# Kernel optimization log

Measured on AMD Instinct MI355X. Metric: run time of the kernel, lower is better.

The kernel has to match this reference:

```python
import jax, jax.numpy as jnp
import numpy as np

B, H = 2048, 1024
P_DROP = 0.6


def setup_inputs() -> dict:
    key = jax.random.key(0)
    ks = jax.random.split(key, 17)
    stdv = 1.0 / np.sqrt(H)
    u = lambda k, shape: jax.random.uniform(k, shape, jnp.float32, -stdv, stdv)
    inp = {
        'input': jax.random.normal(ks[0], (B, H), jnp.float32),
        'hidden': jax.random.normal(ks[1], (B, H), jnp.float32),
        'pre_cell': jax.random.normal(ks[2], (B, H), jnp.float32),
        # weights are (hidden_size, input_size) and used as input @ W (requires H == input_size)
        'w_i': u(ks[3], (H, H)), 'w_f': u(ks[4], (H, H)),
        'w_o': u(ks[5], (H, H)), 'w_c': u(ks[6], (H, H)),
        'u_i': u(ks[7], (H, H)), 'u_f': u(ks[8], (H, H)),
        'u_o': u(ks[9], (H, H)), 'u_c': u(ks[10], (H, H)),
        'bias1': u(ks[11], (H,)), 'bias2': u(ks[12], (H,)),
        'bias3': u(ks[13], (H,)), 'bias4': u(ks[14], (H,)),
    }
    # F.dropout(training=True) mask, pre-scaled by 1/(1-p); shape matches h_t [B,1,H]
    keep = jax.random.bernoulli(ks[15], 1.0 - P_DROP, (B, 1, H))
    inp['drop_mask'] = keep.astype(jnp.float32) / (1.0 - P_DROP)
    return inp


def reference(input, hidden, pre_cell, w_i, w_f, w_o, w_c, u_i, u_f, u_o, u_c,
              bias1, bias2, bias3, bias4, drop_mask):
    # Fuse the 8 small GEMMs into 2 big ones: gate order (f, i, o, c)
    Wx = jnp.concatenate([w_f, w_i, w_o, w_c], axis=1)   # [H, 4H]
    Wh = jnp.concatenate([u_f, u_i, u_o, u_c], axis=1)   # [H, 4H]
    b = jnp.concatenate([bias1, bias2, bias3, bias4])    # [4H]
    gates = input @ Wx + hidden @ Wh + b                 # [B, 4H]
    f_t, i_t, o_t, g_t = jnp.split(gates, 4, axis=1)
    f_t = jax.nn.sigmoid(f_t)
    i_t = jax.nn.sigmoid(i_t)
    o_t = jax.nn.sigmoid(o_t)
    g_t = jnp.tanh(g_t)
    c_t = pre_cell * f_t + i_t * g_t                     # [B, H]
    h_t = o_t * jnp.tanh(c_t)                            # [B, H]
    h_t = h_t[:, None, :] * drop_mask                    # dropout (training=True)
    c_t = c_t[:, None, :]
    return h_t, c_t
```

## Files before the change

### kernel.cpp

```cpp
#include <hip/hip_runtime.h>
#include <hip/hip_bf16.h>
#include <cstdint>

#define B_DIM 2048
#define H_DIM 1024
#define K_DIM 2048
#define N_DIM 4096

typedef unsigned short u16;
typedef __attribute__((ext_vector_type(8))) short bf16x8;
typedef __attribute__((ext_vector_type(8))) unsigned short u16x8;
typedef __attribute__((ext_vector_type(4))) float f32x4;

__device__ __forceinline__ u16 f2bf(float f) {
    unsigned int u = __float_as_uint(f);
    u += 0x7FFFu + ((u >> 16) & 1u);
    return (u16)(u >> 16);
}

__device__ __forceinline__ float sigmoid_f(float x) {
    return 1.0f / (1.0f + __expf(-x));
}

__device__ __forceinline__ float tanh_f(float x) {
    float e = __expf(2.0f * x);
    return 1.0f - 2.0f / (e + 1.0f);
}

__device__ __forceinline__ void async16(const u16* g, u16* l) {
    __builtin_amdgcn_global_load_lds(
        (const __attribute__((address_space(1))) unsigned int*)g,
        (__attribute__((address_space(3))) unsigned int*)l,
        16, 0, 0);
}

__global__ __launch_bounds__(256) void pack_all(
    const float* __restrict__ input, const float* __restrict__ hidden,
    const float* __restrict__ w_f, const float* __restrict__ w_i,
    const float* __restrict__ w_o, const float* __restrict__ w_c,
    const float* __restrict__ u_f, const float* __restrict__ u_i,
    const float* __restrict__ u_o, const float* __restrict__ u_c,
    const float* __restrict__ b1, const float* __restrict__ b2,
    const float* __restrict__ b3, const float* __restrict__ b4,
    u16* __restrict__ A, u16* __restrict__ Bt, float* __restrict__ bias_il) {
    __shared__ float tile[32][65];
    const int blk = blockIdx.x;
    const int t = threadIdx.x;

    if (blk < 4096) {
        int idx = (blk * 256 + t) * 4;
        int m = idx >> 11;
        int k = idx & (K_DIM - 1);
        const float* src = (k < H_DIM) ? (input + (size_t)m * H_DIM + k)
                                       : (hidden + (size_t)m * H_DIM + (k - H_DIM));
        float4 v = *(const float4*)src;
        ushort4 o;
        o.x = f2bf(v.x); o.y = f2bf(v.y); o.z = f2bf(v.z); o.w = f2bf(v.w);
        *(ushort4*)(A + idx) = o;
    } else if (blk < 8192) {
        int b2i = blk - 4096;
        int z = b2i >> 9;
        int rem = b2i & 511;
        int hx = rem & 31;
        int ky = rem >> 5;
        const float* M;
        switch (z) {
            case 0: M = w_f; break;
            case 1: M = w_i; break;
            case 2: M = w_o; break;
            case 3: M = w_c; break;
            case 4: M = u_f; break;
            case 5: M = u_i; break;
            case 6: M = u_o; break;
            default: M = u_c; break;
        }
        const int g = z & 3;
        const int half = z >> 2;
        const int h0 = hx * 32;
        const int k0 = ky * 64;
#pragma unroll
        for (int it = 0; it < 2; it++) {
            int kl = (t >> 3) + it * 32;
            int hl = (t & 7) * 4;
            float4 v = *(const float4*)(M + (size_t)(k0 + kl) * H_DIM + h0 + hl);
            tile[hl + 0][kl] = v.x;
            tile[hl + 1][kl] = v.y;
            tile[hl + 2][kl] = v.z;
            tile[hl + 3][kl] = v.w;
        }
        __syncthreads();
        int hl = t >> 3;
        int ko = (t & 7) * 8;
        u16x8 o;
#pragma unroll
        for (int q = 0; q < 8; q++) o[q] = f2bf(tile[hl][ko + q]);
        size_t n = 4 * (size_t)(h0 + hl) + g;
        *(u16x8*)(Bt + n * K_DIM + half * H_DIM + k0 + ko) = o;
    } else {
        int idx = (blk - 8192) * 256 + t;
        int h = idx >> 2, g = idx & 3;
        const float* b = (g == 0) ? b1 : (g == 1) ? b2 : (g == 2) ? b3 : b4;
        bias_il[idx] = b[h];
    }
}

#define BM 128
#define BN 128

__global__ __launch_bounds__(256, 2) void gemm_fused(
    const u16* __restrict__ A, const u16* __restrict__ Bt,
    const float* __restrict__ bias_il, const float* __restrict__ pre_cell,
    const float* __restrict__ mask, float* __restrict__ out) {
    __shared__ char smem[65536];
    float* et = (float*)smem;

    const int t = threadIdx.x;
    const int w = t >> 6, l = t & 63;
    const int m0 = blockIdx.y * BM;
    const int n0 = blockIdx.x * BN;
    const int wr = w >> 1;
    const int wc = w & 1;
    const int lrow = l & 15;
    const int quad = l >> 4;

    const int srow = t >> 2;
    const int skswz = ((t & 3) * 8) ^ ((srow & 6) << 2);
    const u16* AgS0 = A + (size_t)(m0 + srow) * K_DIM + skswz;
    const u16* AgS1 = AgS0 + (size_t)64 * K_DIM;
    const u16* BgS0 = Bt + (size_t)(n0 + srow) * K_DIM + skswz;
    const u16* BgS1 = BgS0 + (size_t)64 * K_DIM;

    const int swzf = (quad * 8) ^ ((lrow & 6) << 2);
    const int foA = (wr * 64 + lrow) * 32 + swzf;
    const int foB = (wc * 64 + lrow) * 32 + swzf;

    f32x4 acc[4][4];
#pragma unroll
    for (int j = 0; j < 4; j++) {
        float bv = bias_il[n0 + wc * 64 + j * 16 + lrow];
#pragma unroll
        for (int i = 0; i < 4; i++) acc[i][j] = (f32x4){bv, bv, bv, bv};
    }
    asm volatile("s_waitcnt vmcnt(0)" ::: "memory");

#define STAGE(p)                                                            \
    {                                                                       \
        u16* As_ = (u16*)(smem + ((p) & 3) * 16384);                        \
        u16* Bs_ = As_ + 4096;                                              \
        const int ko_ = (p) * 32;                                           \
        async16(AgS0 + ko_, As_ + t * 8);                                   \
        async16(AgS1 + ko_, As_ + 2048 + t * 8);                            \
        async16(BgS0 + ko_, Bs_ + t * 8);                                   \
        async16(BgS1 + ko_, Bs_ + 2048 + t * 8);                            \
    }

    STAGE(0); STAGE(1); STAGE(2);

#define KSTEP(kt, DO_STAGE, VM)                                             \
    {                                                                       \
        asm volatile("s_waitcnt vmcnt(" #VM ")" ::: "memory");              \
        __builtin_amdgcn_s_barrier();                                       \
        asm volatile("" ::: "memory");                                      \
        if (DO_STAGE) STAGE((kt) + 3);                                      \
        const u16* As = (const u16*)(smem + ((kt) & 3) * 16384);            \
        const u16* Bs = As + 4096;                                          \
        bf16x8 af[4], bf[4];                                                \
        _Pragma("unroll") for (int i = 0; i < 4; i++)                       \
            af[i] = *(const bf16x8*)(As + foA + i * 512);                   \
        _Pragma("unroll") for (int j = 0; j < 4; j++)                       \
            bf[j] = *(const bf16x8*)(Bs + foB + j * 512);                   \
        __builtin_amdgcn_s_setprio(1);                                      \
        _Pragma("unroll") for (int i = 0; i < 4; i++)                       \
            _Pragma("unroll") for (int j = 0; j < 4; j++)                   \
                acc[i][j] = __builtin_amdgcn_mfma_f32_16x16x32_bf16(        \
                    af[i], bf[j], acc[i][j], 0, 0, 0);                      \
        __builtin_amdgcn_s_setprio(0);                                      \
        asm volatile("" ::: "memory");                                      \
    }

    for (int kt = 0; kt < 60; kt += 4) {
        KSTEP(kt + 0, true, 8);
        KSTEP(kt + 1, true, 8);
        KSTEP(kt + 2, true, 8);
        KSTEP(kt + 3, true, 8);
    }
    KSTEP(60, true, 8);
    KSTEP(61, false, 8);
    KSTEP(62, false, 4);
    KSTEP(63, false, 0);
#undef KSTEP
#undef STAGE

    const int row = t >> 1;
    const int half = t & 1;
    const size_t orow = (size_t)(m0 + row) * H_DIM;

    float4 pc[4], mk[4];
#pragma unroll
    for (int j = 0; j < 4; j++) {
        const int hg0 = (n0 >> 2) + half * 16 + j * 4;
        pc[j] = *(const float4*)(pre_cell + orow + hg0);
        mk[j] = *(const float4*)(mask + orow + hg0);
    }

#pragma unroll
    for (int j = 0; j < 4; j++) {
        __syncthreads();
#pragma unroll
        for (int i = 0; i < 4; i++)
#pragma unroll
            for (int r = 0; r < 4; r++)
                et[(wr * 64 + i * 16 + quad * 4 + r) * 33 + wc * 16 + lrow] =
                    acc[i][j][r];
        __syncthreads();
        const int hg0 = (n0 >> 2) + half * 16 + j * 4;
        const float* ep = et + row * 33 + half * 16;
        const float* ppc = (const float*)&pc[j];
        const float* pmk = (const float*)&mk[j];
        float4 oh, oc;
        float* poh = (float*)&oh;
        float* poc = (float*)&oc;
#pragma unroll
        for (int q = 0; q < 4; q++) {
            float fv = sigmoid_f(ep[4 * q + 0]);
            float iv = sigmoid_f(ep[4 * q + 1]);
            float ov = sigmoid_f(ep[4 * q + 2]);
            float gv = tanh_f(ep[4 * q + 3]);
            float cv = ppc[q] * fv + iv * gv;
            poc[q] = cv;
            poh[q] = ov * tanh_f(cv) * pmk[q];
        }
        *(float4*)(out + orow + hg0) = oh;
        *(float4*)(out + (size_t)B_DIM * H_DIM + orow + hg0) = oc;
    }
}

extern "C" void kernel_launch(void* const* d_in, const int* in_sizes, int n_in,
                              void* d_out, int out_size, void* d_ws, size_t ws_size,
                              hipStream_t stream) {
    const float* input    = (const float*)d_in[0];
    const float* hidden   = (const float*)d_in[1];
    const float* pre_cell = (const float*)d_in[2];
    const float* w_i = (const float*)d_in[3];
    const float* w_f = (const float*)d_in[4];
    const float* w_o = (const float*)d_in[5];
    const float* w_c = (const float*)d_in[6];
    const float* u_i = (const float*)d_in[7];
    const float* u_f = (const float*)d_in[8];
    const float* u_o = (const float*)d_in[9];
    const float* u_c = (const float*)d_in[10];
    const float* b1  = (const float*)d_in[11];
    const float* b2  = (const float*)d_in[12];
    const float* b3  = (const float*)d_in[13];
    const float* b4  = (const float*)d_in[14];
    const float* mask = (const float*)d_in[15];
    float* out = (float*)d_out;

    char* ws = (char*)d_ws;
    u16*   A       = (u16*)ws;
    u16*   Bt      = (u16*)(ws + (size_t)8 * 1024 * 1024);
    float* bias_il = (float*)(ws + (size_t)24 * 1024 * 1024);

    pack_all<<<dim3(4096 + 4096 + 16), dim3(256), 0, stream>>>(
        input, hidden, w_f, w_i, w_o, w_c, u_f, u_i, u_o, u_c,
        b1, b2, b3, b4, A, Bt, bias_il);
    gemm_fused<<<dim3(N_DIM / BN, B_DIM / BM), dim3(256), 0, stream>>>(
        A, Bt, bias_il, pre_cell, mask, out);
}
```

Before: 169.2 us.

## Pre-pack B into MFMA fragment order and load directly to registers

The weight pack kernel now writes B in a fragment-tiled layout, so each lane's 16-byte MFMA operand is contiguous per k-step. The GEMM then loads B straight from global memory into registers with inline asm and double buffers them in registers (even/odd k-steps), instead of staging B through LDS. This halves LDS usage per block and removes the B LDS reads, which may allow more occupancy. In exchange, the two warps that share a B column tile each fetch it from global/L2, and the hand-counted vmcnt waits must exactly match the in-flight load order.

Result: no change. 168.8 us (-0.2%).

```diff
diff --git a/kernel.cpp b/kernel.cpp
--- a/kernel.cpp
+++ b/kernel.cpp
@@ -42,7 +42,7 @@
     const float* __restrict__ u_o, const float* __restrict__ u_c,
     const float* __restrict__ b1, const float* __restrict__ b2,
     const float* __restrict__ b3, const float* __restrict__ b4,
-    u16* __restrict__ A, u16* __restrict__ Bt, float* __restrict__ bias_il) {
+    u16* __restrict__ A, u16* __restrict__ Bf, float* __restrict__ bias_il) {
     __shared__ float tile[32][65];
     const int blk = blockIdx.x;
     const int t = threadIdx.x;
@@ -95,7 +95,12 @@
 #pragma unroll
         for (int q = 0; q < 8; q++) o[q] = f2bf(tile[hl][ko + q]);
         size_t n = 4 * (size_t)(h0 + hl) + g;
-        *(u16x8*)(Bt + n * K_DIM + half * H_DIM + k0 + ko) = o;
+        int kg = half * H_DIM + k0 + ko;
+        size_t ntile = n >> 4;
+        int nrow = (int)(n & 15);
+        int kt = kg >> 5;
+        int k8 = (kg >> 3) & 3;
+        *(u16x8*)(Bf + ((ntile * 64 + kt) * 64 + (k8 * 16 + nrow)) * 8) = o;
     } else {
         int idx = (blk - 8192) * 256 + t;
         int h = idx >> 2, g = idx & 3;
@@ -108,10 +113,10 @@
 #define BN 128
 
 __global__ __launch_bounds__(256, 2) void gemm_fused(
-    const u16* __restrict__ A, const u16* __restrict__ Bt,
+    const u16* __restrict__ A, const u16* __restrict__ Bf,
     const float* __restrict__ bias_il, const float* __restrict__ pre_cell,
     const float* __restrict__ mask, float* __restrict__ out) {
-    __shared__ char smem[65536];
+    __shared__ char smem[32768];
     float* et = (float*)smem;
 
     const int t = threadIdx.x;
@@ -127,12 +132,11 @@
     const int skswz = ((t & 3) * 8) ^ ((srow & 6) << 2);
     const u16* AgS0 = A + (size_t)(m0 + srow) * K_DIM + skswz;
     const u16* AgS1 = AgS0 + (size_t)64 * K_DIM;
-    const u16* BgS0 = Bt + (size_t)(n0 + srow) * K_DIM + skswz;
-    const u16* BgS1 = BgS0 + (size_t)64 * K_DIM;
 
     const int swzf = (quad * 8) ^ ((lrow & 6) << 2);
     const int foA = (wr * 64 + lrow) * 32 + swzf;
-    const int foB = (wc * 64 + lrow) * 32 + swzf;
+
+    const u16* Bq = Bf + ((size_t)(n0 >> 4) + wc * 4) * 32768 + (size_t)l * 8;
 
     f32x4 acc[4][4];
 #pragma unroll
@@ -143,53 +147,73 @@
     }
     asm volatile("s_waitcnt vmcnt(0)" ::: "memory");
 
-#define STAGE(p)                                                            \
+#define STAGEA(p)                                                           \
     {                                                                       \
-        u16* As_ = (u16*)(smem + ((p) & 3) * 16384);                        \
-        u16* Bs_ = As_ + 4096;                                              \
+        u16* As_ = (u16*)(smem + ((p) & 3) * 8192);                         \
         const int ko_ = (p) * 32;                                           \
         async16(AgS0 + ko_, As_ + t * 8);                                   \
         async16(AgS1 + ko_, As_ + 2048 + t * 8);                            \
-        async16(BgS0 + ko_, Bs_ + t * 8);                                   \
-        async16(BgS1 + ko_, Bs_ + 2048 + t * 8);                            \
-    }
-
-    STAGE(0); STAGE(1); STAGE(2);
-
-#define KSTEP(kt, DO_STAGE, VM)                                             \
+    }
+
+#define LOADB(reg, j, ktt)                                                  \
+    asm volatile("global_load_dwordx4 %0, %1, off"                          \
+                 : "=v"(reg)                                                \
+                 : "v"(Bq + (size_t)(j) * 32768 + (size_t)(ktt) * 512)      \
+                 : "memory");
+
+    bf16x8 bE0, bE1, bE2, bE3, bO0, bO1, bO2, bO3;
+    STAGEA(0); STAGEA(1); STAGEA(2);
+    asm volatile("" ::: "memory");
+    LOADB(bE0, 0, 0); LOADB(bE1, 1, 0); LOADB(bE2, 2, 0); LOADB(bE3, 3, 0);
+    LOADB(bO0, 0, 1); LOADB(bO1, 1, 1); LOADB(bO2, 2, 1); LOADB(bO3, 3, 1);
+
+#define KSTEP(kt, R0, R1, R2, R3, ACNT, BCNT, DOSTAGE, DOLOADB)             \
     {                                                                       \
-        asm volatile("s_waitcnt vmcnt(" #VM ")" ::: "memory");              \
+        asm volatile("s_waitcnt vmcnt(" #ACNT ")" ::: "memory");            \
         __builtin_amdgcn_s_barrier();                                       \
-        asm volatile("" ::: "memory");                                      \
-        if (DO_STAGE) STAGE((kt) + 3);                                      \
-        const u16* As = (const u16*)(smem + ((kt) & 3) * 16384);            \
-        const u16* Bs = As + 4096;                                          \
-        bf16x8 af[4], bf[4];                                                \
+        if (DOSTAGE) STAGEA((kt) + 3);                                      \
+        const u16* As = (const u16*)(smem + ((kt) & 3) * 8192);             \
+        bf16x8 af[4];                                                       \
         _Pragma("unroll") for (int i = 0; i < 4; i++)                       \
             af[i] = *(const bf16x8*)(As + foA + i * 512);                   \
-        _Pragma("unroll") for (int j = 0; j < 4; j++)                       \
-            bf[j] = *(const bf16x8*)(Bs + foB + j * 512);                   \
+        asm volatile("s_waitcnt vmcnt(" #BCNT ")" ::: "memory");            \
+        __builtin_amdgcn_sched_barrier(0);                                  \
         __builtin_amdgcn_s_setprio(1);                                      \
-        _Pragma("unroll") for (int i = 0; i < 4; i++)                       \
-            _Pragma("unroll") for (int j = 0; j < 4; j++)                   \
-                acc[i][j] = __builtin_amdgcn_mfma_f32_16x16x32_bf16(        \
-                    af[i], bf[j], acc[i][j], 0, 0, 0);                      \
+        _Pragma("unroll") for (int i = 0; i < 4; i++) {                     \
+            acc[i][0] = __builtin_amdgcn_mfma_f32_16x16x32_bf16(            \
+                af[i], R0, acc[i][0], 0, 0, 0);                             \
+            acc[i][1] = __builtin_amdgcn_mfma_f32_16x16x32_bf16(            \
+                af[i], R1, acc[i][1], 0, 0, 0);                             \
+            acc[i][2] = __builtin_amdgcn_mfma_f32_16x16x32_bf16(            \
+                af[i], R2, acc[i][2], 0, 0, 0);                             \
+            acc[i][3] = __builtin_amdgcn_mfma_f32_16x16x32_bf16(            \
+                af[i], R3, acc[i][3], 0, 0, 0);                             \
+        }                                                                   \
         __builtin_amdgcn_s_setprio(0);                                      \
+        if (DOLOADB) {                                                      \
+            LOADB(R0, 0, (kt) + 2); LOADB(R1, 1, (kt) + 2);                 \
+            LOADB(R2, 2, (kt) + 2); LOADB(R3, 3, (kt) + 2);                 \
+        }                                                                   \
         asm volatile("" ::: "memory");                                      \
     }
 
-    for (int kt = 0; kt < 60; kt += 4) {
-        KSTEP(kt + 0, true, 8);
-        KSTEP(kt + 1, true, 8);
-        KSTEP(kt + 2, true, 8);
-        KSTEP(kt + 3, true, 8);
-    }
-    KSTEP(60, true, 8);
-    KSTEP(61, false, 8);
-    KSTEP(62, false, 4);
-    KSTEP(63, false, 0);
+    KSTEP(0, bE0, bE1, bE2, bE3, 12, 6, 1, 1);
+    KSTEP(1, bO0, bO1, bO2, bO3, 16, 8, 1, 1);
+    for (int kt = 2; kt < 58; kt += 4) {
+        KSTEP(kt + 0, bE0, bE1, bE2, bE3, 16, 8, 1, 1);
+        KSTEP(kt + 1, bO0, bO1, bO2, bO3, 16, 8, 1, 1);
+        KSTEP(kt + 2, bE0, bE1, bE2, bE3, 16, 8, 1, 1);
+        KSTEP(kt + 3, bO0, bO1, bO2, bO3, 16, 8, 1, 1);
+    }
+    KSTEP(58, bE0, bE1, bE2, bE3, 16, 8, 1, 1);
+    KSTEP(59, bO0, bO1, bO2, bO3, 16, 8, 1, 1);
+    KSTEP(60, bE0, bE1, bE2, bE3, 16, 8, 1, 1);
+    KSTEP(61, bO0, bO1, bO2, bO3, 16, 6, 0, 1);
+    KSTEP(62, bE0, bE1, bE2, bE3, 14, 4, 0, 0);
+    KSTEP(63, bO0, bO1, bO2, bO3,  8, 0, 0, 0);
 #undef KSTEP
-#undef STAGE
+#undef STAGEA
+#undef LOADB
 
     const int row = t >> 1;
     const int half = t & 1;
@@ -258,12 +282,12 @@
 
     char* ws = (char*)d_ws;
     u16*   A       = (u16*)ws;
-    u16*   Bt      = (u16*)(ws + (size_t)8 * 1024 * 1024);
+    u16*   Bf      = (u16*)(ws + (size_t)8 * 1024 * 1024);
     float* bias_il = (float*)(ws + (size_t)24 * 1024 * 1024);
 
     pack_all<<<dim3(4096 + 4096 + 16), dim3(256), 0, stream>>>(
         input, hidden, w_f, w_i, w_o, w_c, u_f, u_i, u_o, u_c,
-        b1, b2, b3, b4, A, Bt, bias_il);
+        b1, b2, b3, b4, A, Bf, bias_il);
     gemm_fused<<<dim3(N_DIM / BN, B_DIM / BM), dim3(256), 0, stream>>>(
-        A, Bt, bias_il, pre_cell, mask, out);
-}
+        A, Bf, bias_il, pre_cell, mask, out);
+}
```
